# Kernel optimization log

Hardware: AMD Instinct MI355X
Metric: run time of the kernel (lower is better)

The kernel has to match this reference:

```python
import jax, jax.numpy as jnp
import numpy as np

D_MODEL = 1024
EXPANSION = 4
NUM_TILES = 4
D_FF = D_MODEL * EXPANSION


def setup_inputs() -> dict:
    key = jax.random.key(0)
    k1, k2, k3, k4, k5 = jax.random.split(key, 5)
    x = jax.random.normal(k1, (8, 2048, D_MODEL), dtype=jnp.float32)
    w_up = jax.random.normal(k2, (D_FF, D_MODEL), dtype=jnp.float32) * 0.02
    b_up = jax.random.normal(k3, (D_FF,), dtype=jnp.float32) * 0.02
    w_down = jax.random.normal(k4, (D_MODEL, D_FF), dtype=jnp.float32) * 0.02
    b_down = jax.random.normal(k5, (D_MODEL,), dtype=jnp.float32) * 0.02
    return {"x": x, "w_up": w_up, "b_up": b_up, "w_down": w_down, "b_down": b_down}


def reference(x, w_up, b_up, w_down, b_down):
    B, T, C = x.shape
    xf = x.reshape(B * T, C)  # [N, d_model]
    N = B * T

    # Emergent tile signatures: sign of per-tile row sums of up_proj weight.
    tile_up = D_FF // NUM_TILES
    signatures = jnp.sign(w_up.reshape(NUM_TILES, tile_up, C).sum(axis=1))  # [num_tiles, d_model]

    # Routing: argmax over input-signature alignment -> one-hot gate.
    scores = xf @ signatures.T                      # [N, num_tiles]
    winner = jnp.argmax(scores, axis=-1)            # [N]
    gate = jax.nn.one_hot(winner, NUM_TILES, dtype=xf.dtype)  # [N, num_tiles]

    # Tile-gated up projection (gate scales output tile blocks), then ReLU.
    hidden = xf @ w_up.T + b_up                     # [N, d_ff]
    hidden = (hidden.reshape(N, NUM_TILES, tile_up) * gate[:, :, None]).reshape(N, D_FF)
    hidden = jax.nn.relu(hidden)

    # Tile-gated down projection.
    tile_down = D_MODEL // NUM_TILES
    out = hidden @ w_down.T + b_down                # [N, d_model]
    out = (out.reshape(N, NUM_TILES, tile_down) * gate[:, :, None]).reshape(N, D_MODEL)

    return out.reshape(B, T, D_MODEL), gate.reshape(B, T, NUM_TILES)
```

## Files before the change

### kernel.cpp

```cpp
#include <hip/hip_runtime.h>
#include <stdint.h>
#include <stddef.h>

#define N_TOK 16384
#define DM    1024
#define DFF   4096
#define NT    4
#define TU    1024
#define TD    256

typedef __attribute__((ext_vector_type(8))) short  short8;
typedef __attribute__((ext_vector_type(4))) short  short4v;
typedef __attribute__((ext_vector_type(4))) float  floatx4;

__device__ inline unsigned short f2bf(float f){
  union { float f; uint32_t u; } v; v.f = f;
  uint32_t u = v.u + 0x7FFFu + ((v.u >> 16) & 1u);
  return (unsigned short)(u >> 16);
}

__device__ __forceinline__ void gll16(const void* g, void* l){
  __builtin_amdgcn_global_load_lds(
      (const __attribute__((address_space(1))) unsigned int*)g,
      (__attribute__((address_space(3))) unsigned int*)l,
      16, 0, 0);
}

__global__ void k_prep(const float* __restrict__ w_up,
                       float* __restrict__ partial,
                       unsigned short* __restrict__ wupb){
  const int tid = threadIdx.x;
  const int b = blockIdx.x;
  const int tile = b >> 6, chunk = b & 63;
  const int c0 = tid * 4;
  const int row0 = tile*TU + chunk*16;
  float s0=0.f, s1=0.f, s2=0.f, s3=0.f;
  const float* base = w_up + (size_t)row0 * DM + c0;
  #pragma unroll
  for (int r = 0; r < 16; ++r){
    floatx4 v = *(const floatx4*)(base + (size_t)r * DM);
    s0 += v[0]; s1 += v[1]; s2 += v[2]; s3 += v[3];
    short4v p;
    p[0]=(short)f2bf(v[0]); p[1]=(short)f2bf(v[1]);
    p[2]=(short)f2bf(v[2]); p[3]=(short)f2bf(v[3]);
    *(short4v*)(wupb + (size_t)(row0 + r) * DM + c0) = p;
  }
  float* p = partial + ((size_t)tile*DM + c0) * 64 + chunk;
  p[0] = s0; p[64] = s1; p[128] = s2; p[192] = s3;
}

__global__ void k_sig_final(const float* __restrict__ partial,
                            float* __restrict__ sig,
                            int* __restrict__ blk_cnt){
  if (blockIdx.x == 0) blk_cnt[threadIdx.x] = 0;
  const int g = blockIdx.x * 256 + threadIdx.x;
  const float* p = partial + (size_t)g * 64;
  float s = 0.f;
  #pragma unroll
  for (int i = 0; i < 64; ++i) s += p[i];
  sig[g] = (s > 0.f) ? 1.f : ((s < 0.f) ? -1.f : 0.f);
}

__global__ __launch_bounds__(256) void k_route(
    const float* __restrict__ x, const float* __restrict__ sig,
    const float* __restrict__ w_down, unsigned short* __restrict__ wdownb,
    float* __restrict__ gate_out, int* __restrict__ winner,
    int* __restrict__ blk_cnt, unsigned short* __restrict__ xbf){
  const int tid = threadIdx.x;
  if (blockIdx.x >= 1024){
    const size_t i = ((size_t)(blockIdx.x - 1024) * 256 + tid) * 8;
    floatx4 v0 = *(const floatx4*)(w_down + i);
    floatx4 v1 = *(const floatx4*)(w_down + i + 4);
    short8 p;
    p[0]=(short)f2bf(v0[0]); p[1]=(short)f2bf(v0[1]); p[2]=(short)f2bf(v0[2]); p[3]=(short)f2bf(v0[3]);
    p[4]=(short)f2bf(v1[0]); p[5]=(short)f2bf(v1[1]); p[6]=(short)f2bf(v1[2]); p[7]=(short)f2bf(v1[3]);
    *(short8*)(wdownb + i) = p;
    return;
  }
  __shared__ float ssig[NT * DM];
  __shared__ int swin[16];
  for (int i = tid; i < NT*DM; i += 256) ssig[i] = sig[i];
  __syncthreads();
  const int wv = tid >> 6, lane = tid & 63;

  floatx4 sg[4][4];
  #pragma unroll
  for (int j = 0; j < 4; ++j){
    const int c = j*256 + lane*4;
    #pragma unroll
    for (int tt = 0; tt < 4; ++tt)
      sg[j][tt] = *(const floatx4*)(ssig + tt*DM + c);
  }

  #pragma unroll
  for (int t = 0; t < 4; ++t){
    const int n = blockIdx.x * 16 + wv * 4 + t;
    const float* xr = x + (size_t)n * DM;
    unsigned short* xb = xbf + (size_t)n * 2048 + 1024;
    double a0=0.0, a1=0.0, a2=0.0, a3=0.0;
    #pragma unroll
    for (int j = 0; j < 4; ++j){
      const int c = j*256 + lane*4;
      floatx4 v = *(const floatx4*)(xr + c);
      short4v p;
      p[0]=(short)f2bf(v[0]); p[1]=(short)f2bf(v[1]);
      p[2]=(short)f2bf(v[2]); p[3]=(short)f2bf(v[3]);
      *(short4v*)(xb + c) = p;
      #pragma unroll
      for (int u = 0; u < 4; ++u){
        double xv = (double)v[u];
        a0 += xv * (double)sg[j][0][u];
        a1 += xv * (double)sg[j][1][u];
        a2 += xv * (double)sg[j][2][u];
        a3 += xv * (double)sg[j][3][u];
      }
    }
    #pragma unroll
    for (int off = 32; off > 0; off >>= 1){
      a0 += __shfl_down(a0, off, 64);
      a1 += __shfl_down(a1, off, 64);
      a2 += __shfl_down(a2, off, 64);
      a3 += __shfl_down(a3, off, 64);
    }
    if (lane == 0){
      double s[4] = {a0, a1, a2, a3};
      int w = 0;
      #pragma unroll
      for (int tt = 1; tt < 4; ++tt) if (s[tt] > s[w]) w = tt;
      floatx4 g = { w==0 ? 1.f:0.f, w==1 ? 1.f:0.f, w==2 ? 1.f:0.f, w==3 ? 1.f:0.f };
      *(floatx4*)(gate_out + (size_t)n * 4) = g;
      winner[n] = w;
      swin[wv*4 + t] = w;
    }
  }
  __syncthreads();
  if (tid < NT){
    int c = 0;
    #pragma unroll
    for (int i = 0; i < 16; ++i) c += (swin[i] == tid) ? 1 : 0;
    if (c) atomicAdd(&blk_cnt[(blockIdx.x >> 4) * NT + tid], c);
  }
}

__global__ void k_scan(const int* __restrict__ blk_cnt,
                       int* __restrict__ meta, int* __restrict__ blk_base){
  __shared__ int s[256];
  const int tid = threadIdx.x;
  s[tid] = blk_cnt[tid];
  __syncthreads();
  if (tid == 0){
    int tot[NT] = {0,0,0,0};
    for (int b = 0; b < 64; ++b)
      for (int t = 0; t < NT; ++t) tot[t] += s[b*NT + t];
    int off = 0, base[NT];
    for (int t = 0; t < NT; ++t){ meta[t] = tot[t]; meta[4+t] = off; base[t] = off; off += tot[t]; }
    for (int b = 0; b < 64; ++b)
      for (int t = 0; t < NT; ++t){ int c = s[b*NT + t]; s[b*NT + t] = base[t]; base[t] += c; }
  }
  __syncthreads();
  blk_base[tid] = s[tid];
}

__global__ void k_scatter(const int* __restrict__ winner,
                          const int* __restrict__ blk_base,
                          int* __restrict__ idx){
  __shared__ int wcnt[4][NT];
  const int tid = threadIdx.x, wv = tid >> 6, lane = tid & 63;
  const int n = blockIdx.x * 256 + tid;
  const int w = winner[n];
  unsigned long long mymask = 0;
  #pragma unroll
  for (int t = 0; t < NT; ++t){
    unsigned long long m = __ballot(w == t);
    if (lane == 0) wcnt[wv][t] = __popcll(m);
    if (t == w) mymask = m;
  }
  __syncthreads();
  const unsigned long long below = (lane == 0) ? 0ull : (~0ull >> (64 - lane));
  int pos = blk_base[blockIdx.x * NT + w] + __popcll(mymask & below);
  for (int v = 0; v < wv; ++v) pos += wcnt[v][w];
  idx[pos] = n;
}

__global__ __launch_bounds__(256, 2) void k_gemm1(
    const unsigned short* __restrict__ xbf,
    const unsigned short* __restrict__ wupb,
    const float* __restrict__ b_up, const int* __restrict__ meta,
    const int* __restrict__ idx, unsigned short* __restrict__ hid){
  const int lin  = blockIdx.x;
  const int r    = lin & 7, q = lin >> 3;
  const int tile = r >> 1;
  const int nb   = q & 7;
  const int chunk = ((q >> 3) << 1) | (r & 1);
  const int p0   = chunk * 128;

  const int cnt  = meta[tile];
  if (p0 >= cnt) return;
  const int off  = meta[4 + tile];

  __shared__ unsigned short smem[16384];
  unsigned short* As0 = smem;
  unsigned short* As1 = smem + 4096;
  unsigned short* Bs0 = smem + 8192;
  unsigned short* Bs1 = smem + 12288;

  const int tid = threadIdx.x;
  const int wv = tid >> 6, lane = tid & 63;
  const int wm = (wv >> 1) * 64, wn = (wv & 1) * 64;
  const int l16 = lane & 15, quad = lane >> 4;
  const int rsub = lane >> 2;
  const int kusw = (((lane & 3) ^ ((lane >> 3) & 3)) * 8);
  const int sq8  = (quad ^ ((l16 >> 1) & 3)) * 8;

  int* nrs = (int*)smem;
  if (tid < 128){
    int p = p0 + tid;
    nrs[tid] = idx[off + (p < cnt ? p : cnt - 1)];
  }
  __syncthreads();
  const int ra = wv*32 + rsub;
  const unsigned short* aptr0 = xbf + (size_t)nrs[ra]      * 2048 + 1024 + kusw;
  const unsigned short* aptr1 = xbf + (size_t)nrs[ra + 16] * 2048 + 1024 + kusw;
  int  enr[2][4];
  bool ev [2][4];
  #pragma unroll
  for (int half = 0; half < 2; ++half){
    #pragma unroll
    for (int s = 0; s < 4; ++s){
      const int lrow = (tid + s*256) >> 4;
      const int m = half*64 + lrow;
      ev [half][s] = (p0 + m < cnt);
      enr[half][s] = nrs[m];
    }
  }
  __syncthreads();

  const unsigned short* bptr0 = wupb + (size_t)(tile*TU + nb*128 + wv*32 + rsub) * DM + kusw;
  const unsigned short* bptr1 = bptr0 + 16 * DM;

  unsigned short* a0d0 = As0 + (wv*32) * 32;  unsigned short* a0d1 = a0d0 + 16*32;
  unsigned short* a1d0 = As1 + (wv*32) * 32;  unsigned short* a1d1 = a1d0 + 16*32;
  unsigned short* b0d0 = Bs0 + (wv*32) * 32;  unsigned short* b0d1 = b0d0 + 16*32;
  unsigned short* b1d0 = Bs1 + (wv*32) * 32;  unsigned short* b1d1 = b1d0 + 16*32;

  floatx4 acc[4][4];
  #pragma unroll
  for (int i = 0; i < 4; ++i)
    #pragma unroll
    for (int j = 0; j < 4; ++j) acc[i][j] = (floatx4){0.f,0.f,0.f,0.f};

  for (int k0 = 0; k0 < DM; k0 += 64){
    gll16(aptr0 + k0,      a0d0);
    gll16(aptr1 + k0,      a0d1);
    gll16(aptr0 + k0 + 32, a1d0);
    gll16(aptr1 + k0 + 32, a1d1);
    gll16(bptr0 + k0,      b0d0);
    gll16(bptr1 + k0,      b0d1);
    gll16(bptr0 + k0 + 32, b1d0);
    gll16(bptr1 + k0 + 32, b1d1);
    __syncthreads();
    {
      short8 af[4], bfr[4];
      #pragma unroll
      for (int i = 0; i < 4; ++i) af[i]  = *(const short8*)(As0 + (wm + i*16 + l16)*32 + sq8);
      #pragma unroll
      for (int j = 0; j < 4; ++j) bfr[j] = *(const short8*)(Bs0 + (wn + j*16 + l16)*32 + sq8);
      #pragma unroll
      for (int i = 0; i < 4; ++i)
        #pragma unroll
        for (int j = 0; j < 4; ++j)
          acc[i][j] = __builtin_amdgcn_mfma_f32_16x16x32_bf16(af[i], bfr[j], acc[i][j], 0, 0, 0);
    }
    {
      short8 af[4], bfr[4];
      #pragma unroll
      for (int i = 0; i < 4; ++i) af[i]  = *(const short8*)(As1 + (wm + i*16 + l16)*32 + sq8);
      #pragma unroll
      for (int j = 0; j < 4; ++j) bfr[j] = *(const short8*)(Bs1 + (wn + j*16 + l16)*32 + sq8);
      #pragma unroll
      for (int i = 0; i < 4; ++i)
        #pragma unroll
        for (int j = 0; j < 4; ++j)
          acc[i][j] = __builtin_amdgcn_mfma_f32_16x16x32_bf16(af[i], bfr[j], acc[i][j], 0, 0, 0);
    }
    __syncthreads();
  }

  const int gcol0 = nb*128;
  #pragma unroll
  for (int half = 0; half < 2; ++half){
    if ((wv >> 1) == half){
      #pragma unroll
      for (int i = 0; i < 4; ++i){
        #pragma unroll
        for (int j = 0; j < 4; ++j){
          const int col = wn + j*16 + l16;
          const float bias = b_up[tile*TU + gcol0 + col];
          #pragma unroll
          for (int r2 = 0; r2 < 4; ++r2){
            const int lrow = i*16 + quad*4 + r2;
            float v = acc[i][j][r2] + bias;
            smem[lrow*136 + col] = f2bf(v > 0.f ? v : 0.f);
          }
        }
      }
    }
    __syncthreads();
    #pragma unroll
    for (int s = 0; s < 4; ++s){
      const int c = tid + s*256;
      const int lrow = c >> 4, k8 = (c & 15) * 8;
      if (ev[half][s]){
        short8 vv = *(const short8*)(smem + lrow*136 + k8);
        *(short8*)(hid + (size_t)enr[half][s]*2048 + gcol0 + k8) = vv;
      }
    }
    __syncthreads();
  }
}

__global__ __launch_bounds__(256, 2) void k_gemm2(
    const unsigned short* __restrict__ hid,
    const unsigned short* __restrict__ wdownb,
    const float* __restrict__ b_down, const int* __restrict__ meta,
    const int* __restrict__ idx, float* __restrict__ out){
  const int lin  = blockIdx.x;
  const int r    = lin & 7, q = lin >> 3;
  const int tile = r >> 1;
  const int xx   = (q << 1) | (r & 1);
  const int p0   = xx * 32;

  const int cnt  = meta[tile];
  if (p0 >= cnt) return;
  const int off  = meta[4 + tile];

  __shared__ unsigned short smem[18432];
  unsigned short* As0 = smem;
  unsigned short* As1 = smem + 1024;
  unsigned short* Bs0 = smem + 2048;
  unsigned short* Bs1 = smem + 10240;
  float* epi = (float*)smem;
  __shared__ int nrow[32];

  const int tid = threadIdx.x;
  if (tid < 32){
    int p = p0 + tid;
    nrow[tid] = idx[off + (p < cnt ? p : cnt - 1)];
  }
  __syncthreads();

  const int wv = tid >> 6, lane = tid & 63;
  const int wn = wv * 64;
  const int l16 = lane & 15, quad = lane >> 4;
  const int rsub = lane >> 2;
  const int kusw = (((lane & 3) ^ ((lane >> 3) & 3)) * 8);
  const int sq8  = (quad ^ ((l16 >> 1) & 3)) * 8;

  const int arow = (wv & 1)*16 + rsub;
  const unsigned short* aptr = hid + (size_t)nrow[arow] * 2048 + kusw;
  const int aoff = (wv >> 1) * 32;
  unsigned short* asd = (wv < 2 ? As0 : As1) + ((wv & 1)*16) * 32;
  const unsigned short* bptr = wdownb + (size_t)(tile*TD + wv*64 + rsub) * DFF + tile*TU + kusw;
  unsigned short* bsd0 = Bs0 + (wv*64) * 32;
  unsigned short* bsd1 = Bs1 + (wv*64) * 32;

  floatx4 acc[2][4];
  #pragma unroll
  for (int i = 0; i < 2; ++i)
    #pragma unroll
    for (int j = 0; j < 4; ++j) acc[i][j] = (floatx4){0.f,0.f,0.f,0.f};

  for (int k0 = 0; k0 < TU; k0 += 64){
    gll16(aptr + k0 + aoff, asd);
    gll16(bptr + k0,               bsd0);
    gll16(bptr + k0 + 16*DFF,      bsd0 + 16*32);
    gll16(bptr + k0 + 32*DFF,      bsd0 + 32*32);
    gll16(bptr + k0 + 48*DFF,      bsd0 + 48*32);
    gll16(bptr + k0 + 32,          bsd1);
    gll16(bptr + k0 + 32 + 16*DFF, bsd1 + 16*32);
    gll16(bptr + k0 + 32 + 32*DFF, bsd1 + 32*32);
    gll16(bptr + k0 + 32 + 48*DFF, bsd1 + 48*32);
    __syncthreads();
    {
      short8 af[2], bfr[4];
      #pragma unroll
      for (int i = 0; i < 2; ++i) af[i]  = *(const short8*)(As0 + (i*16 + l16)*32 + sq8);
      #pragma unroll
      for (int j = 0; j < 4; ++j) bfr[j] = *(const short8*)(Bs0 + (wn + j*16 + l16)*32 + sq8);
      #pragma unroll
      for (int i = 0; i < 2; ++i)
        #pragma unroll
        for (int j = 0; j < 4; ++j)
          acc[i][j] = __builtin_amdgcn_mfma_f32_16x16x32_bf16(af[i], bfr[j], acc[i][j], 0, 0, 0);
    }
    {
      short8 af[2], bfr[4];
      #pragma unroll
      for (int i = 0; i < 2; ++i) af[i]  = *(const short8*)(As1 + (i*16 + l16)*32 + sq8);
      #pragma unroll
      for (int j = 0; j < 4; ++j) bfr[j] = *(const short8*)(Bs1 + (wn + j*16 + l16)*32 + sq8);
      #pragma unroll
      for (int i = 0; i < 2; ++i)
        #pragma unroll
        for (int j = 0; j < 4; ++j)
          acc[i][j] = __builtin_amdgcn_mfma_f32_16x16x32_bf16(af[i], bfr[j], acc[i][j], 0, 0, 0);
    }
    __syncthreads();
  }

  const floatx4 z4 = {0.f, 0.f, 0.f, 0.f};
  #pragma unroll
  for (int cb = 0; cb < 4; ++cb){
    if (cb == tile) continue;
    for (int c = tid; c < 32*64; c += 256){
      const int rowl = c >> 6, c4 = (c & 63) * 4;
      if (p0 + rowl < cnt)
        *(floatx4*)(out + (size_t)nrow[rowl]*DM + cb*256 + c4) = z4;
    }
  }

  #pragma unroll
  for (int half = 0; half < 2; ++half){
    #pragma unroll
    for (int j = 0; j < 4; ++j){
      const int col = wn + j*16 + l16;
      const float bias = b_down[tile*TD + col];
      #pragma unroll
      for (int r2 = 0; r2 < 4; ++r2){
        const int lrow = quad*4 + r2;
        epi[lrow*260 + col] = acc[half][j][r2] + bias;
      }
    }
    __syncthreads();
    #pragma unroll
    for (int c = tid; c < 1024; c += 256){
      const int lrow = c >> 6, c4 = (c & 63) * 4;
      const int m = half*16 + lrow;
      if (p0 + m < cnt){
        floatx4 v = *(const floatx4*)(epi + lrow*260 + c4);
        *(floatx4*)(out + (size_t)nrow[m]*DM + tile*TD + c4) = v;
      }
    }
    __syncthreads();
  }
}

extern "C" void kernel_launch(void* const* d_in, const int* in_sizes, int n_in,
                              void* d_out, int out_size, void* d_ws, size_t ws_size,
                              hipStream_t stream){
  const float* x      = (const float*)d_in[0];
  const float* w_up   = (const float*)d_in[1];
  const float* b_up   = (const float*)d_in[2];
  const float* w_down = (const float*)d_in[3];
  const float* b_down = (const float*)d_in[4];

  unsigned short* wupb   = (unsigned short*)d_ws;
  unsigned short* wdownb = wupb + (size_t)DFF * DM;
  float* partial = (float*)(wdownb + (size_t)DM * DFF);
  float* sig     = partial + 262144;
  int*   ints    = (int*)(sig + 4096);
  int*   winner   = ints;
  int*   idx      = ints + 16384;
  int*   meta     = ints + 32768;
  int*   blk_cnt  = ints + 32776;
  int*   blk_base = ints + 33032;

  float*          out  = (float*)d_out;
  float*          gate = out + (size_t)N_TOK * DM;
  unsigned short* ob16 = (unsigned short*)d_out;

  k_prep      <<<dim3(256),  256, 0, stream>>>(w_up, partial, wupb);
  k_sig_final <<<dim3(16),   256, 0, stream>>>(partial, sig, blk_cnt);
  k_route     <<<dim3(3072), 256, 0, stream>>>(x, sig, w_down, wdownb, gate, winner, blk_cnt, ob16);
  k_scan      <<<dim3(1),    256, 0, stream>>>(blk_cnt, meta, blk_base);
  k_scatter   <<<dim3(64),   256, 0, stream>>>(winner, blk_base, idx);
  k_gemm1     <<<dim3(4096), 256, 0, stream>>>(ob16, wupb, b_up, meta, idx, ob16);
  k_gemm2     <<<dim3(2048), 256, 0, stream>>>(ob16, wdownb, b_down, meta, idx, out);
}
```

Before: 253.9 us.

## Retile down-projection GEMM to 64x128 blocks with 2x2 warp layout

The k_gemm2 block tile changes from 32 tokens x 256 output columns to 64 tokens x 128 columns, with the N dimension split into two panels chosen from the block index. Warps are arranged 2x2 over the tile, which rebalances A and B loads per k-step and shrinks shared memory so more blocks can be resident. The epilogue is restructured to match the new tile shape. A-row gather reuse rises, but each block now covers half the output columns, so the gathered hidden rows are read twice.

```diff
diff --git a/kernel.cpp b/kernel.cpp
--- a/kernel.cpp
+++ b/kernel.cpp
@@ -327,42 +327,39 @@
   const int lin  = blockIdx.x;
   const int r    = lin & 7, q = lin >> 3;
   const int tile = r >> 1;
-  const int xx   = (q << 1) | (r & 1);
-  const int p0   = xx * 32;
+  const int pnl  = q & 1;
+  const int chunk = ((q >> 1) << 1) | (r & 1);
+  const int p0   = chunk * 64;
 
   const int cnt  = meta[tile];
   if (p0 >= cnt) return;
   const int off  = meta[4 + tile];
 
-  __shared__ unsigned short smem[18432];
-  unsigned short* As0 = smem;
-  unsigned short* As1 = smem + 1024;
-  unsigned short* Bs0 = smem + 2048;
-  unsigned short* Bs1 = smem + 10240;
+  __shared__ unsigned short smem[12288];
   float* epi = (float*)smem;
-  __shared__ int nrow[32];
+  __shared__ int nrow[64];
 
   const int tid = threadIdx.x;
-  if (tid < 32){
+  if (tid < 64){
     int p = p0 + tid;
     nrow[tid] = idx[off + (p < cnt ? p : cnt - 1)];
   }
   __syncthreads();
 
   const int wv = tid >> 6, lane = tid & 63;
-  const int wn = wv * 64;
+  const int wr = wv >> 1, wc = wv & 1;
   const int l16 = lane & 15, quad = lane >> 4;
   const int rsub = lane >> 2;
   const int kusw = (((lane & 3) ^ ((lane >> 3) & 3)) * 8);
   const int sq8  = (quad ^ ((l16 >> 1) & 3)) * 8;
 
-  const int arow = (wv & 1)*16 + rsub;
-  const unsigned short* aptr = hid + (size_t)nrow[arow] * 2048 + kusw;
-  const int aoff = (wv >> 1) * 32;
-  unsigned short* asd = (wv < 2 ? As0 : As1) + ((wv & 1)*16) * 32;
-  const unsigned short* bptr = wdownb + (size_t)(tile*TD + wv*64 + rsub) * DFF + tile*TU + kusw;
-  unsigned short* bsd0 = Bs0 + (wv*64) * 32;
-  unsigned short* bsd1 = Bs1 + (wv*64) * 32;
+  const unsigned short* aptr = hid + (size_t)nrow[wv*16 + rsub] * 2048 + kusw;
+  unsigned short* const asd0 = smem + (wv*16) * 32;
+  unsigned short* const asd1 = asd0 + 2048;
+  const unsigned short* bptr = wdownb + (size_t)(tile*TD + pnl*128 + wv*32 + rsub) * DFF
+                                      + tile*TU + kusw;
+  unsigned short* const bsd0 = smem + 4096 + (wv*32) * 32;
+  unsigned short* const bsd1 = bsd0 + 4096;
 
   floatx4 acc[2][4];
   #pragma unroll
@@ -371,22 +368,19 @@
     for (int j = 0; j < 4; ++j) acc[i][j] = (floatx4){0.f,0.f,0.f,0.f};
 
   for (int k0 = 0; k0 < TU; k0 += 64){
-    gll16(aptr + k0 + aoff, asd);
+    gll16(aptr + k0,               asd0);
+    gll16(aptr + k0 + 32,          asd1);
     gll16(bptr + k0,               bsd0);
-    gll16(bptr + k0 + 16*DFF,      bsd0 + 16*32);
-    gll16(bptr + k0 + 32*DFF,      bsd0 + 32*32);
-    gll16(bptr + k0 + 48*DFF,      bsd0 + 48*32);
+    gll16(bptr + k0 + 16*DFF,      bsd0 + 512);
     gll16(bptr + k0 + 32,          bsd1);
-    gll16(bptr + k0 + 32 + 16*DFF, bsd1 + 16*32);
-    gll16(bptr + k0 + 32 + 32*DFF, bsd1 + 32*32);
-    gll16(bptr + k0 + 32 + 48*DFF, bsd1 + 48*32);
+    gll16(bptr + k0 + 32 + 16*DFF, bsd1 + 512);
     __syncthreads();
     {
       short8 af[2], bfr[4];
       #pragma unroll
-      for (int i = 0; i < 2; ++i) af[i]  = *(const short8*)(As0 + (i*16 + l16)*32 + sq8);
-      #pragma unroll
-      for (int j = 0; j < 4; ++j) bfr[j] = *(const short8*)(Bs0 + (wn + j*16 + l16)*32 + sq8);
+      for (int i = 0; i < 2; ++i) af[i]  = *(const short8*)(smem + (wr*32 + i*16 + l16)*32 + sq8);
+      #pragma unroll
+      for (int j = 0; j < 4; ++j) bfr[j] = *(const short8*)(smem + 4096 + (wc*64 + j*16 + l16)*32 + sq8);
       #pragma unroll
       for (int i = 0; i < 2; ++i)
         #pragma unroll
@@ -396,9 +390,9 @@
     {
       short8 af[2], bfr[4];
       #pragma unroll
-      for (int i = 0; i < 2; ++i) af[i]  = *(const short8*)(As1 + (i*16 + l16)*32 + sq8);
-      #pragma unroll
-      for (int j = 0; j < 4; ++j) bfr[j] = *(const short8*)(Bs1 + (wn + j*16 + l16)*32 + sq8);
+      for (int i = 0; i < 2; ++i) af[i]  = *(const short8*)(smem + 2048 + (wr*32 + i*16 + l16)*32 + sq8);
+      #pragma unroll
+      for (int j = 0; j < 4; ++j) bfr[j] = *(const short8*)(smem + 8192 + (wc*64 + j*16 + l16)*32 + sq8);
       #pragma unroll
       for (int i = 0; i < 2; ++i)
         #pragma unroll
@@ -412,33 +406,39 @@
   #pragma unroll
   for (int cb = 0; cb < 4; ++cb){
     if (cb == tile) continue;
-    for (int c = tid; c < 32*64; c += 256){
-      const int rowl = c >> 6, c4 = (c & 63) * 4;
+    for (int c = tid; c < 64*32; c += 256){
+      const int rowl = c >> 5, c4 = (c & 31) * 4;
       if (p0 + rowl < cnt)
-        *(floatx4*)(out + (size_t)nrow[rowl]*DM + cb*256 + c4) = z4;
-    }
-  }
-
-  #pragma unroll
-  for (int half = 0; half < 2; ++half){
-    #pragma unroll
-    for (int j = 0; j < 4; ++j){
-      const int col = wn + j*16 + l16;
-      const float bias = b_down[tile*TD + col];
-      #pragma unroll
-      for (int r2 = 0; r2 < 4; ++r2){
-        const int lrow = quad*4 + r2;
-        epi[lrow*260 + col] = acc[half][j][r2] + bias;
+        *(floatx4*)(out + (size_t)nrow[rowl]*DM + cb*256 + pnl*128 + c4) = z4;
+    }
+  }
+
+  const int gcol0 = tile*TD + pnl*128;
+  #pragma unroll
+  for (int h = 0; h < 2; ++h){
+    if (wr == h){
+      #pragma unroll
+      for (int i = 0; i < 2; ++i){
+        #pragma unroll
+        for (int j = 0; j < 4; ++j){
+          const int col = wc*64 + j*16 + l16;
+          const float bias = b_down[gcol0 + col];
+          #pragma unroll
+          for (int r2 = 0; r2 < 4; ++r2){
+            const int lrow = i*16 + quad*4 + r2;
+            epi[lrow*132 + col] = acc[i][j][r2] + bias;
+          }
+        }
       }
     }
     __syncthreads();
     #pragma unroll
     for (int c = tid; c < 1024; c += 256){
-      const int lrow = c >> 6, c4 = (c & 63) * 4;
-      const int m = half*16 + lrow;
+      const int lrow = c >> 5, c4 = (c & 31) * 4;
+      const int m = h*32 + lrow;
       if (p0 + m < cnt){
-        floatx4 v = *(const floatx4*)(epi + lrow*260 + c4);
-        *(floatx4*)(out + (size_t)nrow[m]*DM + tile*TD + c4) = v;
+        floatx4 v = *(const floatx4*)(epi + lrow*132 + c4);
+        *(floatx4*)(out + (size_t)nrow[m]*DM + gcol0 + c4) = v;
       }
     }
     __syncthreads();
```

Result: faster. 243.0 us (-4.3%).
